# Optimization experiments

Measured on AMD Instinct MI355X. Metric: run time of the kernel, lower is better.

## Reference

```python
import jax, jax.numpy as jnp
import numpy as np

ALPHA = 0.25
GAMMA = 2.0
EPS = 1e-8
W_CLASS = 2.0
W_BBOX = 5.0
W_GIOU = 2.0
B, Q, T, C = 64, 900, 300, 80


def setup_inputs() -> dict:
    key = jax.random.key(0)
    k1, k2, k3, k4 = jax.random.split(key, 4)
    pred_logits = jax.random.normal(k1, (B, Q, C), dtype=jnp.float32)
    pred_boxes = jax.random.uniform(k2, (B, Q, 4), dtype=jnp.float32)  # cxcywh in (0,1)
    tgt_labels = jax.random.randint(k3, (B, T), 0, C, dtype=jnp.int64)
    tgt_boxes = jax.random.uniform(k4, (B, T, 4), dtype=jnp.float32)
    return {"pred_logits": pred_logits, "pred_boxes": pred_boxes,
            "tgt_labels": tgt_labels, "tgt_boxes": tgt_boxes}


def box_cxcywh_to_xyxy(b):
    cx, cy, w, h = b[..., 0], b[..., 1], b[..., 2], b[..., 3]
    return jnp.stack([cx - 0.5 * w, cy - 0.5 * h, cx + 0.5 * w, cy + 0.5 * h], axis=-1)


def pairwise_giou(boxes1, boxes2):
    # boxes1: [B,Q,4] xyxy, boxes2: [B,T,4] xyxy -> [B,Q,T]
    area1 = (boxes1[..., 2] - boxes1[..., 0]) * (boxes1[..., 3] - boxes1[..., 1])
    area2 = (boxes2[..., 2] - boxes2[..., 0]) * (boxes2[..., 3] - boxes2[..., 1])
    lt = jnp.maximum(boxes1[:, :, None, :2], boxes2[:, None, :, :2])
    rb = jnp.minimum(boxes1[:, :, None, 2:], boxes2[:, None, :, 2:])
    wh = jnp.clip(rb - lt, 0.0)
    inter = wh[..., 0] * wh[..., 1]
    union = area1[:, :, None] + area2[:, None, :] - inter
    iou = inter / union
    lt_c = jnp.minimum(boxes1[:, :, None, :2], boxes2[:, None, :, :2])
    rb_c = jnp.maximum(boxes1[:, :, None, 2:], boxes2[:, None, :, 2:])
    wh_c = jnp.clip(rb_c - lt_c, 0.0)
    area_c = wh_c[..., 0] * wh_c[..., 1]
    return iou - (area_c - union) / area_c


def reference(pred_logits, pred_boxes, tgt_labels, tgt_boxes):
    # Batched cost matrix of HungarianMatcher (use_focal_loss=True).
    prob = jax.nn.sigmoid(pred_logits)  # [B,Q,C]
    idx = jnp.broadcast_to(tgt_labels[:, None, :], (prob.shape[0], prob.shape[1], tgt_labels.shape[1]))
    p = jnp.take_along_axis(prob, idx.astype(jnp.int32), axis=2)  # [B,Q,T]
    neg_cost = (1.0 - ALPHA) * p ** GAMMA * (-jnp.log(1.0 - p + EPS))
    pos_cost = ALPHA * (1.0 - p) ** GAMMA * (-jnp.log(p + EPS))
    cost_class = pos_cost - neg_cost
    cost_bbox = jnp.abs(pred_boxes[:, :, None, :] - tgt_boxes[:, None, :, :]).sum(-1)
    cost_giou = -pairwise_giou(box_cxcywh_to_xyxy(pred_boxes), box_cxcywh_to_xyxy(tgt_boxes))
    cost = W_BBOX * cost_bbox + W_CLASS * cost_class + W_GIOU * cost_giou
    return jnp.nan_to_num(cost, nan=1.0, posinf=1e6, neginf=-1e6)
```

## Files before the change

### kernel.cpp

```cpp
#include <hip/hip_runtime.h>


constexpr int B = 64, Q = 900, T = 300, C = 80;
constexpr int QTILE = 36;
constexpr int BLOCK = 320;
constexpr int NQ    = QTILE / 4;
constexpr float ALPHA = 0.25f;

__device__ __forceinline__ float fast_rcp(float x) {
    return __builtin_amdgcn_rcpf(x);
}

__device__ __forceinline__ float focal2(float x) {
    float t  = __expf(-x);
    float p  = fast_rcp(1.0f + t);
    float L  = __logf(1.0f + t);
    float xL = x + L;
    float omp = t * p;
    float pos = ALPHA * omp * omp * L;
    float neg = (1.0f - ALPHA) * p * p * xL;
    return fmaf(2.0f, pos - neg, 2.0f);
}

__global__ __launch_bounds__(BLOCK) void matcher_cost_kernel(
    const float* __restrict__ logits,
    const float* __restrict__ pboxes,
    const int*   __restrict__ tlabels,
    const float* __restrict__ tboxes,
    float* __restrict__ out)
{
    __shared__ float  s_cls[QTILE * C];
    __shared__ float4 s_pA[QTILE];
    __shared__ float4 s_pB[QTILE];

    const int bid = blockIdx.x;
    const int b   = bid / (Q / QTILE);
    const int q0  = (bid % (Q / QTILE)) * QTILE;
    const int tid = threadIdx.x;

    if (tid < QTILE) {
        float4 bx = *(const float4*)(pboxes + ((size_t)b * Q + q0 + tid) * 4);
        s_pA[tid] = bx;
        s_pB[tid] = make_float4(bx.x - 0.5f * bx.z, bx.y - 0.5f * bx.w,
                                bx.x + 0.5f * bx.z, bx.y + 0.5f * bx.w);
    }
    {
        const float* lg = logits + ((size_t)b * Q + q0) * C;
        #pragma unroll
        for (int s = 0; s < QTILE * C / BLOCK; ++s)
            s_cls[s * BLOCK + tid] = focal2(lg[s * BLOCK + tid]);
    }

    const int tq = tid / 75;
    const int tt = (tid < T) ? (tid - tq * 75) : 0;

    float4 tb[4];
    int4   lab = make_int4(0, 0, 0, 0);
    if (tid < T) {
        const float4* tbp = (const float4*)(tboxes + ((size_t)b * T + tt * 4) * 4);
        tb[0] = tbp[0]; tb[1] = tbp[1]; tb[2] = tbp[2]; tb[3] = tbp[3];
        lab = *(const int4*)(tlabels + (size_t)b * T + tt * 4);
    }
    float Tcx[4], Tcy[4], Tw[4], Th[4], Tx0[4], Ty0[4], Tx1[4], Ty1[4];
    #pragma unroll
    for (int k = 0; k < 4; ++k) {
        Tcx[k] = tb[k].x; Tcy[k] = tb[k].y; Tw[k] = tb[k].z; Th[k] = tb[k].w;
        Tx0[k] = tb[k].x - 0.5f * tb[k].z; Ty0[k] = tb[k].y - 0.5f * tb[k].w;
        Tx1[k] = tb[k].x + 0.5f * tb[k].z; Ty1[k] = tb[k].y + 0.5f * tb[k].w;
    }

    __syncthreads();

    if (tid >= T) return;

    const float* cls0 = s_cls + tq * C;
    float* op = out + ((size_t)b * Q + q0 + tq) * T + tt * 4;

    #pragma unroll
    for (int j = 0; j < NQ; ++j) {
        const int ql = tq + 4 * j;
        float4 pA = s_pA[ql];
        float4 pB = s_pB[ql];
        float  pa = pA.z * pA.w;
        const float* clsj = cls0 + j * 4 * C;

        float cls_k[4] = { clsj[lab.x], clsj[lab.y], clsj[lab.z], clsj[lab.w] };

        float4 res;
        #pragma unroll
        for (int k = 0; k < 4; ++k) {
            float wi = fminf(pB.z, Tx1[k]) - fmaxf(pB.x, Tx0[k]);
            float hi = fminf(pB.w, Ty1[k]) - fmaxf(pB.y, Ty0[k]);
            float iw = fmaxf(wi, 0.0f), ih = fmaxf(hi, 0.0f);
            float inter = iw * ih;
            float ta  = Tw[k] * Th[k];
            float uni = (pa + ta) - inter;
            float cw  = (pA.z + Tw[k]) - wi;
            float ch  = (pA.w + Th[k]) - hi;
            float ca  = cw * ch;

            float cbbox = (fabsf(pA.x - Tcx[k]) + fabsf(pA.y - Tcy[k])) +
                          (fabsf(pA.z - Tw[k] ) + fabsf(pA.w - Th[k] ));

            float num = fmaf(uni, uni, inter * ca);
            float r   = fast_rcp(uni * ca);
            float c   = fmaf(5.0f, cbbox, cls_k[k]);
            c = fmaf(num * r, -2.0f, c);

            if (c != c) c = 1.0f;

            (&res.x)[k] = c;
        }
        *(float4*)(op + (size_t)(4 * j) * T) = res;
    }
}

extern "C" void kernel_launch(void* const* d_in, const int* in_sizes, int n_in,
                              void* d_out, int out_size, void* d_ws, size_t ws_size,
                              hipStream_t stream) {
    const float* logits  = (const float*)d_in[0];
    const float* pboxes  = (const float*)d_in[1];
    const int*   tlabels = (const int*)  d_in[2];
    const float* tboxes  = (const float*)d_in[3];
    float* out = (float*)d_out;

    dim3 grid(B * (Q / QTILE));
    dim3 block(BLOCK);
    matcher_cost_kernel<<<grid, block, 0, stream>>>(logits, pboxes, tlabels, tboxes, out);
}
```

Measured before the change: 31.02 us.

## Shrink query tile and recompute box terms from corners to cut registers

Reduces the query tile from 36 to 12 rows and the block from 320 to 256 threads, with 3 query rows per pass (225 active threads), and adds a launch bound asking for 8 blocks per CU. Target boxes are kept only as corner coordinates, and width, height and the L1 centre/size distance are rebuilt from corner differences. This frees registers and shared memory to raise occupancy and grows the grid threefold. The cost is more blocks, roughly 12% of threads idle in the compute phase, recomputing target width and height for every query row, and slightly different float rounding in the bbox term.

```diff
diff --git a/kernel.cpp b/kernel.cpp
--- a/kernel.cpp
+++ b/kernel.cpp
@@ -2,9 +2,10 @@
 
 
 constexpr int B = 64, Q = 900, T = 300, C = 80;
-constexpr int QTILE = 36;
-constexpr int BLOCK = 320;
-constexpr int NQ    = QTILE / 4;
+constexpr int QTILE = 12;
+constexpr int BLOCK = 256;
+constexpr int NTQ   = 3;
+constexpr int NQ    = QTILE / NTQ;
 constexpr float ALPHA = 0.25f;
 
 __device__ __forceinline__ float fast_rcp(float x) {
@@ -22,7 +23,7 @@
     return fmaf(2.0f, pos - neg, 2.0f);
 }
 
-__global__ __launch_bounds__(BLOCK) void matcher_cost_kernel(
+__global__ __launch_bounds__(BLOCK, 8) void matcher_cost_kernel(
     const float* __restrict__ logits,
     const float* __restrict__ pboxes,
     const int*   __restrict__ tlabels,
@@ -30,7 +31,6 @@
     float* __restrict__ out)
 {
     __shared__ float  s_cls[QTILE * C];
-    __shared__ float4 s_pA[QTILE];
     __shared__ float4 s_pB[QTILE];
 
     const int bid = blockIdx.x;
@@ -40,78 +40,81 @@
 
     if (tid < QTILE) {
         float4 bx = *(const float4*)(pboxes + ((size_t)b * Q + q0 + tid) * 4);
-        s_pA[tid] = bx;
         s_pB[tid] = make_float4(bx.x - 0.5f * bx.z, bx.y - 0.5f * bx.w,
                                 bx.x + 0.5f * bx.z, bx.y + 0.5f * bx.w);
     }
     {
         const float* lg = logits + ((size_t)b * Q + q0) * C;
-        #pragma unroll
-        for (int s = 0; s < QTILE * C / BLOCK; ++s)
-            s_cls[s * BLOCK + tid] = focal2(lg[s * BLOCK + tid]);
+        for (int i = tid; i < QTILE * C; i += BLOCK)
+            s_cls[i] = focal2(lg[i]);
     }
 
     const int tq = tid / 75;
-    const int tt = (tid < T) ? (tid - tq * 75) : 0;
+    const int tt = tid - tq * 75;
+    const bool active = (tid < NTQ * 75);
 
-    float4 tb[4];
-    int4   lab = make_int4(0, 0, 0, 0);
-    if (tid < T) {
+    float Tx0[4], Ty0[4], Tx1[4], Ty1[4];
+    int lab[4] = {0, 0, 0, 0};
+    if (active) {
         const float4* tbp = (const float4*)(tboxes + ((size_t)b * T + tt * 4) * 4);
-        tb[0] = tbp[0]; tb[1] = tbp[1]; tb[2] = tbp[2]; tb[3] = tbp[3];
-        lab = *(const int4*)(tlabels + (size_t)b * T + tt * 4);
-    }
-    float Tcx[4], Tcy[4], Tw[4], Th[4], Tx0[4], Ty0[4], Tx1[4], Ty1[4];
-    #pragma unroll
-    for (int k = 0; k < 4; ++k) {
-        Tcx[k] = tb[k].x; Tcy[k] = tb[k].y; Tw[k] = tb[k].z; Th[k] = tb[k].w;
-        Tx0[k] = tb[k].x - 0.5f * tb[k].z; Ty0[k] = tb[k].y - 0.5f * tb[k].w;
-        Tx1[k] = tb[k].x + 0.5f * tb[k].z; Ty1[k] = tb[k].y + 0.5f * tb[k].w;
+        int4 lb = *(const int4*)(tlabels + (size_t)b * T + tt * 4);
+        lab[0] = lb.x; lab[1] = lb.y; lab[2] = lb.z; lab[3] = lb.w;
+        #pragma unroll
+        for (int k = 0; k < 4; ++k) {
+            float4 bx = tbp[k];
+            Tx0[k] = bx.x - 0.5f * bx.z; Ty0[k] = bx.y - 0.5f * bx.w;
+            Tx1[k] = bx.x + 0.5f * bx.z; Ty1[k] = bx.y + 0.5f * bx.w;
+        }
     }
 
     __syncthreads();
 
-    if (tid >= T) return;
+    if (!active) return;
 
     const float* cls0 = s_cls + tq * C;
     float* op = out + ((size_t)b * Q + q0 + tq) * T + tt * 4;
 
     #pragma unroll
     for (int j = 0; j < NQ; ++j) {
-        const int ql = tq + 4 * j;
-        float4 pA = s_pA[ql];
-        float4 pB = s_pB[ql];
-        float  pa = pA.z * pA.w;
-        const float* clsj = cls0 + j * 4 * C;
+        float4 pB = s_pB[tq + NTQ * j];
+        float pw = pB.z - pB.x, ph = pB.w - pB.y;
+        float pa = pw * ph;
+        const float* clsj = cls0 + j * NTQ * C;
 
-        float cls_k[4] = { clsj[lab.x], clsj[lab.y], clsj[lab.z], clsj[lab.w] };
+        float cls_k[4] = { clsj[lab[0]], clsj[lab[1]], clsj[lab[2]], clsj[lab[3]] };
 
         float4 res;
         #pragma unroll
         for (int k = 0; k < 4; ++k) {
+            float dx0 = pB.x - Tx0[k], dx1 = pB.z - Tx1[k];
+            float dy0 = pB.y - Ty0[k], dy1 = pB.w - Ty1[k];
+
+            float tw = Tx1[k] - Tx0[k], th = Ty1[k] - Ty0[k];
+            float ta = tw * th;
+
             float wi = fminf(pB.z, Tx1[k]) - fmaxf(pB.x, Tx0[k]);
             float hi = fminf(pB.w, Ty1[k]) - fmaxf(pB.y, Ty0[k]);
             float iw = fmaxf(wi, 0.0f), ih = fmaxf(hi, 0.0f);
             float inter = iw * ih;
-            float ta  = Tw[k] * Th[k];
             float uni = (pa + ta) - inter;
-            float cw  = (pA.z + Tw[k]) - wi;
-            float ch  = (pA.w + Th[k]) - hi;
+            float cw  = (pw + tw) - wi;
+            float ch  = (ph + th) - hi;
             float ca  = cw * ch;
 
-            float cbbox = (fabsf(pA.x - Tcx[k]) + fabsf(pA.y - Tcy[k])) +
-                          (fabsf(pA.z - Tw[k] ) + fabsf(pA.w - Th[k] ));
+            float cb = fabsf(dx1 - dx0) + fabsf(dy1 - dy0);
+            cb = fmaf(0.5f, fabsf(dx0 + dx1), cb);
+            cb = fmaf(0.5f, fabsf(dy0 + dy1), cb);
 
             float num = fmaf(uni, uni, inter * ca);
             float r   = fast_rcp(uni * ca);
-            float c   = fmaf(5.0f, cbbox, cls_k[k]);
+            float c   = fmaf(5.0f, cb, cls_k[k]);
             c = fmaf(num * r, -2.0f, c);
 
             if (c != c) c = 1.0f;
 
             (&res.x)[k] = c;
         }
-        *(float4*)(op + (size_t)(4 * j) * T) = res;
+        *(float4*)(op + (size_t)(NTQ * j) * T) = res;
     }
 }
 
```

Result: slower. 94.76 us (+205.5%).
